# Optimization experiments

Measured on AMD Instinct MI355X. Metric: run time of the kernel, lower is better.

## Reference

```python
import jax, jax.numpy as jnp
import numpy as np

N_EMBD = 448
HEAD_SIZE = 64

def setup_inputs() -> dict:
    key = jax.random.key(0)
    k1, k2, k3, k4 = jax.random.split(key, 4)
    B, T = 16, 2048
    x = jax.random.normal(k1, (B, T, N_EMBD), dtype=jnp.float32)
    # nn.Linear(n_embd, head_size, bias=False): weight shape (head_size, n_embd); y = x @ W.T
    s = 1.0 / np.sqrt(N_EMBD)
    Wk = jax.random.uniform(k2, (HEAD_SIZE, N_EMBD), jnp.float32, -s, s)
    Wq = jax.random.uniform(k3, (HEAD_SIZE, N_EMBD), jnp.float32, -s, s)
    Wv = jax.random.uniform(k4, (HEAD_SIZE, N_EMBD), jnp.float32, -s, s)
    return {"x": x, "Wk": Wk, "Wq": Wq, "Wv": Wv}

def reference(x, Wk, Wq, Wv):
    B, T, C = x.shape
    k = jnp.einsum('btc,hc->bth', x, Wk)  # (B,T,H)
    q = jnp.einsum('btc,hc->bth', x, Wq)
    v = jnp.einsum('btc,hc->bth', x, Wv)
    scale = 1.0 / jnp.sqrt(jnp.float32(C))  # NOTE: scales by sqrt(n_embd), as in source
    wei = jnp.einsum('bth,bsh->bts', q, k) * scale  # (B,T,T)
    causal = jnp.tril(jnp.ones((T, T), dtype=bool))
    wei = jnp.where(causal[None, :, :], wei, -jnp.inf)
    wei = jax.nn.softmax(wei, axis=-1)
    # dropout is identity in eval mode
    out = jnp.einsum('bts,bsh->bth', wei, v)  # (B,T,H)
    return out
```

## Files before the change

kernel.cpp:

```cpp
#include <hip/hip_runtime.h>
#include <math.h>

#define BT 32768
#define NC 448
#define NH 64
#define TT 2048

typedef __bf16 bf16x8 __attribute__((ext_vector_type(8)));
typedef __bf16 bf16x2 __attribute__((ext_vector_type(2)));
typedef float  f32x4  __attribute__((ext_vector_type(4)));

__device__ __forceinline__ unsigned short f2bf(float f) {
  __bf16 h = (__bf16)f;
  return __builtin_bit_cast(unsigned short, h);
}
__device__ __forceinline__ ushort4 f2bf4(float4 v) {
  ushort4 b; b.x = f2bf(v.x); b.y = f2bf(v.y); b.z = f2bf(v.z); b.w = f2bf(v.w);
  return b;
}
__device__ __forceinline__ float bf2f(unsigned short u) {
  return __builtin_bit_cast(float, (unsigned)u << 16);
}


__global__ __launch_bounds__(256) void wprep_kernel(
    const float* __restrict__ Wk, const float* __restrict__ Wq,
    const float* __restrict__ Wv, unsigned short* __restrict__ wp)
{
  int idx = blockIdx.x * 256 + threadIdx.x;
  int r = idx & 63;
  int t = idx >> 6;
  int g = t & 7; t >>= 3;
  int ch = t % 7, p = t / 7;
  const float* W = (p == 0) ? Wk : ((p == 1) ? Wq : Wv);
  const float* src = &W[(size_t)r * NC + ch * 64 + g * 8];
  float4 a = *(const float4*)src;
  float4 b = *(const float4*)(src + 4);
  *(ushort4*)&wp[(size_t)idx * 8]     = f2bf4(a);
  *(ushort4*)&wp[(size_t)idx * 8 + 4] = f2bf4(b);
}

__global__ __launch_bounds__(256) void proj_kernel(
    const float* __restrict__ x, const unsigned short* __restrict__ wp,
    unsigned short* __restrict__ kws, unsigned short* __restrict__ qws,
    unsigned short* __restrict__ vws)
{
  __shared__ unsigned short xs[2][4096];
  const int tid = threadIdx.x;
  const int w = tid >> 6, lane = tid & 63;
  const int q = lane >> 4, l15 = lane & 15;
  const int r0 = blockIdx.x * 64;

  f32x4 acc[3][4];
#pragma unroll
  for (int p = 0; p < 3; ++p)
#pragma unroll
    for (int t = 0; t < 4; ++t) acc[p][t] = f32x4{0.f, 0.f, 0.f, 0.f};

  const int c0 = (tid & 15) * 4, r_ = tid >> 4;
  const int wbase = (w * 16 + l15) * 8;

  float4 xr[4];
  bf16x8 wfr[3][2], wnx[3][2];
#pragma unroll
  for (int i = 0; i < 4; ++i)
    xr[i] = *(const float4*)&x[(size_t)(r0 + r_ + 16 * i) * NC + c0];
#pragma unroll
  for (int p = 0; p < 3; ++p)
#pragma unroll
    for (int ks = 0; ks < 2; ++ks)
      wfr[p][ks] = *(const bf16x8*)&wp[(size_t)((p * 7 + 0) * 8 + (q + 4 * ks)) * 512 + wbase];

  for (int ch = 0; ch < 7; ++ch) {
    const int cur = ch & 1;
#pragma unroll
    for (int i = 0; i < 4; ++i) {
      int r = r_ + 16 * i;
      int off = r * 64 + (((c0 >> 3) ^ (r & 7)) << 3) + (c0 & 7);
      *(ushort4*)&xs[cur][off] = f2bf4(xr[i]);
    }
    __syncthreads();
    if (ch < 6) {
      int kc = (ch + 1) * 64;
#pragma unroll
      for (int i = 0; i < 4; ++i)
        xr[i] = *(const float4*)&x[(size_t)(r0 + r_ + 16 * i) * NC + kc + c0];
#pragma unroll
      for (int p = 0; p < 3; ++p)
#pragma unroll
        for (int ks = 0; ks < 2; ++ks)
          wnx[p][ks] = *(const bf16x8*)&wp[(size_t)((p * 7 + ch + 1) * 8 + (q + 4 * ks)) * 512 + wbase];
    }
#pragma unroll
    for (int ks = 0; ks < 2; ++ks) {
#pragma unroll
      for (int t = 0; t < 4; ++t) {
        int xrow = t * 16 + l15;
        bf16x8 xf = *(const bf16x8*)&xs[cur][xrow * 64 + (((q + 4 * ks) ^ (xrow & 7)) << 3)];
        acc[0][t] = __builtin_amdgcn_mfma_f32_16x16x32_bf16(wfr[0][ks], xf, acc[0][t], 0, 0, 0);
        acc[1][t] = __builtin_amdgcn_mfma_f32_16x16x32_bf16(xf, wfr[1][ks], acc[1][t], 0, 0, 0);
        acc[2][t] = __builtin_amdgcn_mfma_f32_16x16x32_bf16(xf, wfr[2][ks], acc[2][t], 0, 0, 0);
      }
    }
    if (ch < 6) {
#pragma unroll
      for (int p = 0; p < 3; ++p)
#pragma unroll
        for (int ks = 0; ks < 2; ++ks)
          wfr[p][ks] = wnx[p][ks];
    }
  }

  const size_t tile = (size_t)blockIdx.x * 4096;
#pragma unroll
  for (int t = 0; t < 4; ++t) {
    int j = t * 16 + l15;
    ushort4 bb; bb.x = f2bf(acc[0][t][0]); bb.y = f2bf(acc[0][t][1]);
    bb.z = f2bf(acc[0][t][2]); bb.w = f2bf(acc[0][t][3]);
    *(ushort4*)&kws[tile + j * 64 + (((2 * w + (q >> 1)) ^ (j & 7)) << 3) + ((q & 1) << 2)] = bb;
  }
  {
    const float qs = 0.068161075f;
    int h = w * 16 + l15;
#pragma unroll
    for (int t = 0; t < 4; ++t)
#pragma unroll
      for (int rr = 0; rr < 4; ++rr) {
        int R = r0 + t * 16 + q * 4 + rr;
        qws[(size_t)R * 64 + h] = f2bf(acc[1][t][rr] * qs);
      }
  }
  {
    int h = w * 16 + l15;
#pragma unroll
    for (int t = 0; t < 4; ++t) {
      ushort4 bb; bb.x = f2bf(acc[2][t][0]); bb.y = f2bf(acc[2][t][1]);
      bb.z = f2bf(acc[2][t][2]); bb.w = f2bf(acc[2][t][3]);
      *(ushort4*)&vws[tile + h * 64 + (((2 * t + (q >> 1)) ^ (h & 7)) << 3) + ((q & 1) << 2)] = bb;
    }
  }
}

__global__ __launch_bounds__(256) void attn_partial(
    const unsigned short* __restrict__ kws, const unsigned short* __restrict__ qws,
    const unsigned short* __restrict__ vws, float* __restrict__ out,
    unsigned short* __restrict__ opart, float* __restrict__ mlpart)
{
  __shared__ unsigned short ksm[2][4096];
  __shared__ unsigned short vtm[2][4096];
  const int bx = blockIdx.x, b = blockIdx.y;
  int qt = 0, c = 0;
  {
    int idx = bx;
    if (idx < 52) {
      for (int q2 = 31; q2 >= 7; --q2) {
        int L = (q2 + 1) >> 3;
        if (idx < L) { qt = q2; c = idx; break; }
        idx -= L;
      }
    } else {
      idx -= 52;
      for (int q2 = 31; q2 >= 0; --q2) {
        if ((q2 + 1) & 7) {
          if (idx == 0) { qt = q2; c = (q2 + 1) >> 3; break; }
          --idx;
        }
      }
    }
  }
  const int kt0 = c * 8;
  const int ktn = min(kt0 + 8, qt + 1);
  const int nt = ktn - kt0;
  const bool direct = (qt <= 7);

  const int tid = threadIdx.x;
  const int w = tid >> 6, lane = tid & 63;
  const int q = lane >> 4, l15 = lane & 15;
  const int t0 = b * TT + qt * 64;

  bf16x8 qf[2];
#pragma unroll
  for (int ks = 0; ks < 2; ++ks)
    qf[ks] = *(const bf16x8*)&qws[(size_t)(t0 + w * 16 + l15) * 64 + 32 * ks + q * 8];

  f32x4 oacc[4];
#pragma unroll
  for (int ht = 0; ht < 4; ++ht) oacc[ht] = f32x4{0.f, 0.f, 0.f, 0.f};
  float m_i = -INFINITY, l_i = 0.f;

  uint4 kr0, kr1, vr0, vr1;
  {
    const unsigned short* kt_ = kws + (size_t)(b * 32 + kt0) * 4096;
    const unsigned short* vt_ = vws + (size_t)(b * 32 + kt0) * 4096;
    kr0 = *(const uint4*)&kt_[tid * 8];  kr1 = *(const uint4*)&kt_[2048 + tid * 8];
    vr0 = *(const uint4*)&vt_[tid * 8];  vr1 = *(const uint4*)&vt_[2048 + tid * 8];
  }

  const int srcA = (((2 * q) & 3) << 4) + l15;
  const int srcB = (((2 * q + 1) & 3) << 4) + l15;
  const bool hiq = (q >> 1) != 0;

  for (int it = 0; it < nt; ++it) {
    const int kt = kt0 + it;
    const int cur = it & 1;
    *(uint4*)&ksm[cur][tid * 8] = kr0;  *(uint4*)&ksm[cur][2048 + tid * 8] = kr1;
    *(uint4*)&vtm[cur][tid * 8] = vr0;  *(uint4*)&vtm[cur][2048 + tid * 8] = vr1;
    __syncthreads();
    if (it + 1 < nt) {
      const unsigned short* kt_ = kws + (size_t)(b * 32 + kt + 1) * 4096;
      const unsigned short* vt_ = vws + (size_t)(b * 32 + kt + 1) * 4096;
      kr0 = *(const uint4*)&kt_[tid * 8];  kr1 = *(const uint4*)&kt_[2048 + tid * 8];
      vr0 = *(const uint4*)&vt_[tid * 8];  vr1 = *(const uint4*)&vt_[2048 + tid * 8];
    }

    f32x4 sacc[4];
#pragma unroll
    for (int jt = 0; jt < 4; ++jt) sacc[jt] = f32x4{0.f, 0.f, 0.f, 0.f};
    __builtin_amdgcn_s_setprio(1);
#pragma unroll
    for (int jt = 0; jt < 4; ++jt) {
      int j = jt * 16 + l15;
#pragma unroll
      for (int ks = 0; ks < 2; ++ks) {
        bf16x8 kf = *(const bf16x8*)&ksm[cur][j * 64 + (((q + 4 * ks) ^ (j & 7)) << 3)];
        sacc[jt] = __builtin_amdgcn_mfma_f32_16x16x32_bf16(kf, qf[ks], sacc[jt], 0, 0, 0);
      }
    }
    __builtin_amdgcn_s_setprio(0);

    if (kt == qt) {
      int iloc = w * 16 + l15;
#pragma unroll
      for (int jt = 0; jt < 4; ++jt)
#pragma unroll
        for (int rr = 0; rr < 4; ++rr)
          if (jt * 16 + q * 4 + rr > iloc) sacc[jt][rr] = -INFINITY;
    }

    float mx = -INFINITY;
#pragma unroll
    for (int jt = 0; jt < 4; ++jt)
#pragma unroll
      for (int rr = 0; rr < 4; ++rr) mx = fmaxf(mx, sacc[jt][rr]);
    mx = fmaxf(mx, __shfl_xor(mx, 16));
    mx = fmaxf(mx, __shfl_xor(mx, 32));
    if (!__all(mx <= m_i + 11.0f)) {
      float mn = fmaxf(m_i, mx);
      float alpha = exp2f(m_i - mn);
      m_i = mn;
      l_i *= alpha;
      float a_t[4];
#pragma unroll
      for (int rr = 0; rr < 4; ++rr) a_t[rr] = __shfl(alpha, q * 4 + rr);
#pragma unroll
      for (int ht = 0; ht < 4; ++ht)
#pragma unroll
        for (int rr = 0; rr < 4; ++rr) oacc[ht][rr] *= a_t[rr];
    }
    float rs = 0.f;
#pragma unroll
    for (int jt = 0; jt < 4; ++jt)
#pragma unroll
      for (int rr = 0; rr < 4; ++rr) {
        float pv = exp2f(sacc[jt][rr] - m_i);
        sacc[jt][rr] = pv; rs += pv;
      }
    rs += __shfl_xor(rs, 16);
    rs += __shfl_xor(rs, 32);
    l_i += rs;

    unsigned pku[4][2];
#pragma unroll
    for (int jt = 0; jt < 4; ++jt)
#pragma unroll
      for (int h2 = 0; h2 < 2; ++h2) {
        bf16x2 tpk;
        tpk[0] = (__bf16)sacc[jt][2 * h2];
        tpk[1] = (__bf16)sacc[jt][2 * h2 + 1];
        pku[jt][h2] = __builtin_bit_cast(unsigned, tpk);
      }

    __builtin_amdgcn_s_setprio(1);
#pragma unroll
    for (int ks2 = 0; ks2 < 2; ++ks2) {
      unsigned a0 = __shfl(pku[2 * ks2][0], srcA), b0 = __shfl(pku[2 * ks2 + 1][0], srcA);
      unsigned a1 = __shfl(pku[2 * ks2][1], srcA), b1 = __shfl(pku[2 * ks2 + 1][1], srcA);
      unsigned a2 = __shfl(pku[2 * ks2][0], srcB), b2 = __shfl(pku[2 * ks2 + 1][0], srcB);
      unsigned a3 = __shfl(pku[2 * ks2][1], srcB), b3 = __shfl(pku[2 * ks2 + 1][1], srcB);
      uint4 wds;
      wds.x = hiq ? b0 : a0; wds.y = hiq ? b1 : a1;
      wds.z = hiq ? b2 : a2; wds.w = hiq ? b3 : a3;
      bf16x8 pf = __builtin_bit_cast(bf16x8, wds);
#pragma unroll
      for (int ht = 0; ht < 4; ++ht) {
        int h = ht * 16 + l15;
        bf16x8 vf = *(const bf16x8*)&vtm[cur][h * 64 + (((q + 4 * ks2) ^ (h & 7)) << 3)];
        oacc[ht] = __builtin_amdgcn_mfma_f32_16x16x32_bf16(pf, vf, oacc[ht], 0, 0, 0);
      }
    }
    __builtin_amdgcn_s_setprio(0);
  }

  if (direct) {
    float l_t[4];
#pragma unroll
    for (int rr = 0; rr < 4; ++rr) l_t[rr] = __shfl(l_i, q * 4 + rr);
#pragma unroll
    for (int rr = 0; rr < 4; ++rr) {
      float inv = 1.f / l_t[rr];
      int R = t0 + w * 16 + q * 4 + rr;
#pragma unroll
      for (int ht = 0; ht < 4; ++ht)
        out[(size_t)R * 64 + ht * 16 + l15] = oacc[ht][rr] * inv;
    }
  } else {
    const int pre = (qt < 16) ? 2 * (qt - 8) : (qt < 24 ? 16 + 3 * (qt - 16) : 40 + 4 * (qt - 24));
    const size_t slot = (size_t)b * 72 + pre + c;
    unsigned short* Op = opart + slot * 4096;
#pragma unroll
    for (int rr = 0; rr < 4; ++rr) {
      int rloc = w * 16 + q * 4 + rr;
#pragma unroll
      for (int ht = 0; ht < 4; ++ht)
        Op[rloc * 64 + ht * 16 + l15] = f2bf(oacc[ht][rr]);
    }
    if (q == 0) {
      mlpart[slot * 128 + w * 16 + l15]      = m_i;
      mlpart[slot * 128 + 64 + w * 16 + l15] = l_i;
    }
  }
}

__global__ __launch_bounds__(256) void combine_kernel(
    const unsigned short* __restrict__ opart, const float* __restrict__ mlpart,
    float* __restrict__ out)
{
  const int qtc = blockIdx.x, b = blockIdx.y;
  const int qt = 8 + qtc;
  const int nc = (qt >> 3) + 1;
  const int pre = (qt < 16) ? 2 * (qt - 8) : (qt < 24 ? 16 + 3 * (qt - 16) : 40 + 4 * (qt - 24));
  const size_t s0 = (size_t)b * 72 + pre;
  const int t = threadIdx.x;
  const int r = t >> 2, c0 = (t & 3) * 16;

  float m = -INFINITY;
  for (int i = 0; i < nc; ++i)
    m = fmaxf(m, mlpart[(s0 + i) * 128 + r]);
  float wsum = 0.f;
  for (int i = 0; i < nc; ++i)
    wsum += exp2f(mlpart[(s0 + i) * 128 + r] - m) * mlpart[(s0 + i) * 128 + 64 + r];
  const float inv = 1.f / wsum;

  float res[16];
#pragma unroll
  for (int u = 0; u < 16; ++u) res[u] = 0.f;
  for (int i = 0; i < nc; ++i) {
    float wi = exp2f(mlpart[(s0 + i) * 128 + r] - m) * inv;
    const unsigned short* O = opart + (s0 + i) * 4096 + r * 64 + c0;
    union { uint4 v; unsigned short e[8]; } u0, u1;
    u0.v = *(const uint4*)&O[0];
    u1.v = *(const uint4*)&O[8];
#pragma unroll
    for (int u = 0; u < 8; ++u) {
      res[u]     += wi * bf2f(u0.e[u]);
      res[8 + u] += wi * bf2f(u1.e[u]);
    }
  }
  float* op = out + (size_t)(b * TT + qt * 64 + r) * 64 + c0;
  *(float4*)&op[0]  = make_float4(res[0], res[1], res[2], res[3]);
  *(float4*)&op[4]  = make_float4(res[4], res[5], res[6], res[7]);
  *(float4*)&op[8]  = make_float4(res[8], res[9], res[10], res[11]);
  *(float4*)&op[12] = make_float4(res[12], res[13], res[14], res[15]);
}

extern "C" void kernel_launch(void* const* d_in, const int* in_sizes, int n_in,
                              void* d_out, int out_size, void* d_ws, size_t ws_size,
                              hipStream_t stream) {
  const float* x  = (const float*)d_in[0];
  const float* Wk = (const float*)d_in[1];
  const float* Wq = (const float*)d_in[2];
  const float* Wv = (const float*)d_in[3];
  unsigned short* kws = (unsigned short*)d_ws;
  unsigned short* qws = kws + (size_t)BT * NH;
  unsigned short* vws = qws + (size_t)BT * NH;
  unsigned short* opart = vws + (size_t)BT * NH;
  float* mlpart = (float*)(opart + (size_t)1152 * 4096);
  float* out = (float*)d_out;
  unsigned short* wprep = opart;

  wprep_kernel<<<dim3(42), 256, 0, stream>>>(Wk, Wq, Wv, wprep);
  proj_kernel<<<dim3(512), 256, 0, stream>>>(x, wprep, kws, qws, vws);
  attn_partial<<<dim3(80, 16), 256, 0, stream>>>(kws, qws, vws, out, opart, mlpart);
  combine_kernel<<<dim3(24, 16), 256, 0, stream>>>(opart, mlpart, out);
}
```

Baseline: 141.3 us.

## Split attention blocks into single-wave blocks loading K/V fragments directly from global

Each 256-thread attention block becomes four independent 64-thread blocks, one per 16-row query slice. The LDS staging and __syncthreads of K/V tiles are dropped, and each wave loads its MFMA K and V fragments straight from global memory into registers, double-buffered with a ping-pong unrolled loop. The projection kernel now writes K and V without the XOR swizzle to match the new access pattern. This removes block-level barriers and LDS traffic, but each wave now reads whole K/V tiles itself, which quadruples global/L2 reads and raises register pressure.

```diff
diff --git a/kernel.cpp b/kernel.cpp
--- a/kernel.cpp
+++ b/kernel.cpp
@@ -21,7 +21,6 @@
 __device__ __forceinline__ float bf2f(unsigned short u) {
   return __builtin_bit_cast(float, (unsigned)u << 16);
 }
-
 
 __global__ __launch_bounds__(256) void wprep_kernel(
     const float* __restrict__ Wk, const float* __restrict__ Wq,
@@ -117,7 +116,7 @@
     int j = t * 16 + l15;
     ushort4 bb; bb.x = f2bf(acc[0][t][0]); bb.y = f2bf(acc[0][t][1]);
     bb.z = f2bf(acc[0][t][2]); bb.w = f2bf(acc[0][t][3]);
-    *(ushort4*)&kws[tile + j * 64 + (((2 * w + (q >> 1)) ^ (j & 7)) << 3) + ((q & 1) << 2)] = bb;
+    *(ushort4*)&kws[tile + j * 64 + w * 16 + 4 * q] = bb;
   }
   {
     const float qs = 0.068161075f;
@@ -136,22 +135,121 @@
     for (int t = 0; t < 4; ++t) {
       ushort4 bb; bb.x = f2bf(acc[2][t][0]); bb.y = f2bf(acc[2][t][1]);
       bb.z = f2bf(acc[2][t][2]); bb.w = f2bf(acc[2][t][3]);
-      *(ushort4*)&vws[tile + h * 64 + (((2 * t + (q >> 1)) ^ (h & 7)) << 3) + ((q & 1) << 2)] = bb;
-    }
-  }
-}
-
-__global__ __launch_bounds__(256) void attn_partial(
+      *(ushort4*)&vws[tile + h * 64 + t * 16 + 4 * q] = bb;
+    }
+  }
+}
+
+__device__ __forceinline__ void attn_iter(
+    bf16x8 (&kc)[4][2], bf16x8 (&vc)[4][2],
+    bf16x8 (&kn)[4][2], bf16x8 (&vn)[4][2],
+    int it, int nt, bool isdiag,
+    const unsigned short* __restrict__ kbn, const unsigned short* __restrict__ vbn,
+    const bf16x8 (&qf)[2], f32x4 (&oacc)[4],
+    float& m_i, float& l_i,
+    int q, int l15, int wv, int srcA, int srcB, bool hiq)
+{
+  if (it + 1 < nt) {
+#pragma unroll
+    for (int jt = 0; jt < 4; ++jt)
+#pragma unroll
+      for (int ks = 0; ks < 2; ++ks) {
+        kn[jt][ks] = *(const bf16x8*)&kbn[(jt * 16 + l15) * 64 + (q + 4 * ks) * 8];
+        vn[jt][ks] = *(const bf16x8*)&vbn[(jt * 16 + l15) * 64 + (q + 4 * ks) * 8];
+      }
+  }
+
+  f32x4 sacc[4];
+#pragma unroll
+  for (int jt = 0; jt < 4; ++jt) sacc[jt] = f32x4{0.f, 0.f, 0.f, 0.f};
+  __builtin_amdgcn_s_setprio(1);
+#pragma unroll
+  for (int jt = 0; jt < 4; ++jt)
+#pragma unroll
+    for (int ks = 0; ks < 2; ++ks)
+      sacc[jt] = __builtin_amdgcn_mfma_f32_16x16x32_bf16(kc[jt][ks], qf[ks], sacc[jt], 0, 0, 0);
+  __builtin_amdgcn_s_setprio(0);
+
+  if (isdiag) {
+    int iloc = wv * 16 + l15;
+#pragma unroll
+    for (int jt = 0; jt < 4; ++jt)
+#pragma unroll
+      for (int rr = 0; rr < 4; ++rr)
+        if (jt * 16 + q * 4 + rr > iloc) sacc[jt][rr] = -INFINITY;
+  }
+
+  float mx = -INFINITY;
+#pragma unroll
+  for (int jt = 0; jt < 4; ++jt)
+#pragma unroll
+    for (int rr = 0; rr < 4; ++rr) mx = fmaxf(mx, sacc[jt][rr]);
+  mx = fmaxf(mx, __shfl_xor(mx, 16));
+  mx = fmaxf(mx, __shfl_xor(mx, 32));
+  if (!__all(mx <= m_i + 11.0f)) {
+    float mn = fmaxf(m_i, mx);
+    float alpha = exp2f(m_i - mn);
+    m_i = mn;
+    l_i *= alpha;
+    float a_t[4];
+#pragma unroll
+    for (int rr = 0; rr < 4; ++rr) a_t[rr] = __shfl(alpha, q * 4 + rr);
+#pragma unroll
+    for (int ht = 0; ht < 4; ++ht)
+#pragma unroll
+      for (int rr = 0; rr < 4; ++rr) oacc[ht][rr] *= a_t[rr];
+  }
+  float rs = 0.f;
+#pragma unroll
+  for (int jt = 0; jt < 4; ++jt)
+#pragma unroll
+    for (int rr = 0; rr < 4; ++rr) {
+      float pv = exp2f(sacc[jt][rr] - m_i);
+      sacc[jt][rr] = pv; rs += pv;
+    }
+  rs += __shfl_xor(rs, 16);
+  rs += __shfl_xor(rs, 32);
+  l_i += rs;
+
+  unsigned pku[4][2];
+#pragma unroll
+  for (int jt = 0; jt < 4; ++jt)
+#pragma unroll
+    for (int h2 = 0; h2 < 2; ++h2) {
+      bf16x2 tpk;
+      tpk[0] = (__bf16)sacc[jt][2 * h2];
+      tpk[1] = (__bf16)sacc[jt][2 * h2 + 1];
+      pku[jt][h2] = __builtin_bit_cast(unsigned, tpk);
+    }
+
+  __builtin_amdgcn_s_setprio(1);
+#pragma unroll
+  for (int ks2 = 0; ks2 < 2; ++ks2) {
+    unsigned a0 = __shfl(pku[2 * ks2][0], srcA), b0 = __shfl(pku[2 * ks2 + 1][0], srcA);
+    unsigned a1 = __shfl(pku[2 * ks2][1], srcA), b1 = __shfl(pku[2 * ks2 + 1][1], srcA);
+    unsigned a2 = __shfl(pku[2 * ks2][0], srcB), b2 = __shfl(pku[2 * ks2 + 1][0], srcB);
+    unsigned a3 = __shfl(pku[2 * ks2][1], srcB), b3 = __shfl(pku[2 * ks2 + 1][1], srcB);
+    uint4 wds;
+    wds.x = hiq ? b0 : a0; wds.y = hiq ? b1 : a1;
+    wds.z = hiq ? b2 : a2; wds.w = hiq ? b3 : a3;
+    bf16x8 pf = __builtin_bit_cast(bf16x8, wds);
+#pragma unroll
+    for (int ht = 0; ht < 4; ++ht)
+      oacc[ht] = __builtin_amdgcn_mfma_f32_16x16x32_bf16(pf, vc[ht][ks2], oacc[ht], 0, 0, 0);
+  }
+  __builtin_amdgcn_s_setprio(0);
+}
+
+__global__ __launch_bounds__(64, 2) void attn_partial(
     const unsigned short* __restrict__ kws, const unsigned short* __restrict__ qws,
     const unsigned short* __restrict__ vws, float* __restrict__ out,
     unsigned short* __restrict__ opart, float* __restrict__ mlpart)
 {
-  __shared__ unsigned short ksm[2][4096];
-  __shared__ unsigned short vtm[2][4096];
   const int bx = blockIdx.x, b = blockIdx.y;
+  const int cid = bx >> 2, wv = bx & 3;
   int qt = 0, c = 0;
   {
-    int idx = bx;
+    int idx = cid;
     if (idx < 52) {
       for (int q2 = 31; q2 >= 7; --q2) {
         int L = (q2 + 1) >> 3;
@@ -173,132 +271,44 @@
   const int nt = ktn - kt0;
   const bool direct = (qt <= 7);
 
-  const int tid = threadIdx.x;
-  const int w = tid >> 6, lane = tid & 63;
+  const int lane = threadIdx.x & 63;
   const int q = lane >> 4, l15 = lane & 15;
   const int t0 = b * TT + qt * 64;
 
   bf16x8 qf[2];
 #pragma unroll
   for (int ks = 0; ks < 2; ++ks)
-    qf[ks] = *(const bf16x8*)&qws[(size_t)(t0 + w * 16 + l15) * 64 + 32 * ks + q * 8];
+    qf[ks] = *(const bf16x8*)&qws[(size_t)(t0 + wv * 16 + l15) * 64 + 32 * ks + q * 8];
 
   f32x4 oacc[4];
 #pragma unroll
   for (int ht = 0; ht < 4; ++ht) oacc[ht] = f32x4{0.f, 0.f, 0.f, 0.f};
   float m_i = -INFINITY, l_i = 0.f;
-
-  uint4 kr0, kr1, vr0, vr1;
-  {
-    const unsigned short* kt_ = kws + (size_t)(b * 32 + kt0) * 4096;
-    const unsigned short* vt_ = vws + (size_t)(b * 32 + kt0) * 4096;
-    kr0 = *(const uint4*)&kt_[tid * 8];  kr1 = *(const uint4*)&kt_[2048 + tid * 8];
-    vr0 = *(const uint4*)&vt_[tid * 8];  vr1 = *(const uint4*)&vt_[2048 + tid * 8];
-  }
 
   const int srcA = (((2 * q) & 3) << 4) + l15;
   const int srcB = (((2 * q + 1) & 3) << 4) + l15;
   const bool hiq = (q >> 1) != 0;
 
-  for (int it = 0; it < nt; ++it) {
-    const int kt = kt0 + it;
-    const int cur = it & 1;
-    *(uint4*)&ksm[cur][tid * 8] = kr0;  *(uint4*)&ksm[cur][2048 + tid * 8] = kr1;
-    *(uint4*)&vtm[cur][tid * 8] = vr0;  *(uint4*)&vtm[cur][2048 + tid * 8] = vr1;
-    __syncthreads();
-    if (it + 1 < nt) {
-      const unsigned short* kt_ = kws + (size_t)(b * 32 + kt + 1) * 4096;
-      const unsigned short* vt_ = vws + (size_t)(b * 32 + kt + 1) * 4096;
-      kr0 = *(const uint4*)&kt_[tid * 8];  kr1 = *(const uint4*)&kt_[2048 + tid * 8];
-      vr0 = *(const uint4*)&vt_[tid * 8];  vr1 = *(const uint4*)&vt_[2048 + tid * 8];
-    }
-
-    f32x4 sacc[4];
-#pragma unroll
-    for (int jt = 0; jt < 4; ++jt) sacc[jt] = f32x4{0.f, 0.f, 0.f, 0.f};
-    __builtin_amdgcn_s_setprio(1);
-#pragma unroll
-    for (int jt = 0; jt < 4; ++jt) {
-      int j = jt * 16 + l15;
-#pragma unroll
-      for (int ks = 0; ks < 2; ++ks) {
-        bf16x8 kf = *(const bf16x8*)&ksm[cur][j * 64 + (((q + 4 * ks) ^ (j & 7)) << 3)];
-        sacc[jt] = __builtin_amdgcn_mfma_f32_16x16x32_bf16(kf, qf[ks], sacc[jt], 0, 0, 0);
-      }
-    }
-    __builtin_amdgcn_s_setprio(0);
-
-    if (kt == qt) {
-      int iloc = w * 16 + l15;
-#pragma unroll
-      for (int jt = 0; jt < 4; ++jt)
-#pragma unroll
-        for (int rr = 0; rr < 4; ++rr)
-          if (jt * 16 + q * 4 + rr > iloc) sacc[jt][rr] = -INFINITY;
-    }
-
-    float mx = -INFINITY;
-#pragma unroll
-    for (int jt = 0; jt < 4; ++jt)
-#pragma unroll
-      for (int rr = 0; rr < 4; ++rr) mx = fmaxf(mx, sacc[jt][rr]);
-    mx = fmaxf(mx, __shfl_xor(mx, 16));
-    mx = fmaxf(mx, __shfl_xor(mx, 32));
-    if (!__all(mx <= m_i + 11.0f)) {
-      float mn = fmaxf(m_i, mx);
-      float alpha = exp2f(m_i - mn);
-      m_i = mn;
-      l_i *= alpha;
-      float a_t[4];
-#pragma unroll
-      for (int rr = 0; rr < 4; ++rr) a_t[rr] = __shfl(alpha, q * 4 + rr);
-#pragma unroll
-      for (int ht = 0; ht < 4; ++ht)
-#pragma unroll
-        for (int rr = 0; rr < 4; ++rr) oacc[ht][rr] *= a_t[rr];
-    }
-    float rs = 0.f;
-#pragma unroll
-    for (int jt = 0; jt < 4; ++jt)
-#pragma unroll
-      for (int rr = 0; rr < 4; ++rr) {
-        float pv = exp2f(sacc[jt][rr] - m_i);
-        sacc[jt][rr] = pv; rs += pv;
-      }
-    rs += __shfl_xor(rs, 16);
-    rs += __shfl_xor(rs, 32);
-    l_i += rs;
-
-    unsigned pku[4][2];
-#pragma unroll
-    for (int jt = 0; jt < 4; ++jt)
-#pragma unroll
-      for (int h2 = 0; h2 < 2; ++h2) {
-        bf16x2 tpk;
-        tpk[0] = (__bf16)sacc[jt][2 * h2];
-        tpk[1] = (__bf16)sacc[jt][2 * h2 + 1];
-        pku[jt][h2] = __builtin_bit_cast(unsigned, tpk);
-      }
-
-    __builtin_amdgcn_s_setprio(1);
-#pragma unroll
-    for (int ks2 = 0; ks2 < 2; ++ks2) {
-      unsigned a0 = __shfl(pku[2 * ks2][0], srcA), b0 = __shfl(pku[2 * ks2 + 1][0], srcA);
-      unsigned a1 = __shfl(pku[2 * ks2][1], srcA), b1 = __shfl(pku[2 * ks2 + 1][1], srcA);
-      unsigned a2 = __shfl(pku[2 * ks2][0], srcB), b2 = __shfl(pku[2 * ks2 + 1][0], srcB);
-      unsigned a3 = __shfl(pku[2 * ks2][1], srcB), b3 = __shfl(pku[2 * ks2 + 1][1], srcB);
-      uint4 wds;
-      wds.x = hiq ? b0 : a0; wds.y = hiq ? b1 : a1;
-      wds.z = hiq ? b2 : a2; wds.w = hiq ? b3 : a3;
-      bf16x8 pf = __builtin_bit_cast(bf16x8, wds);
-#pragma unroll
-      for (int ht = 0; ht < 4; ++ht) {
-        int h = ht * 16 + l15;
-        bf16x8 vf = *(const bf16x8*)&vtm[cur][h * 64 + (((q + 4 * ks2) ^ (h & 7)) << 3)];
-        oacc[ht] = __builtin_amdgcn_mfma_f32_16x16x32_bf16(pf, vf, oacc[ht], 0, 0, 0);
-      }
-    }
-    __builtin_amdgcn_s_setprio(0);
+  const unsigned short* kb0 = kws + (size_t)(b * 32 + kt0) * 4096;
+  const unsigned short* vb0 = vws + (size_t)(b * 32 + kt0) * 4096;
+
+  bf16x8 kA[4][2], vA[4][2], kB[4][2], vB[4][2];
+#pragma unroll
+  for (int jt = 0; jt < 4; ++jt)
+#pragma unroll
+    for (int ks = 0; ks < 2; ++ks) {
+      kA[jt][ks] = *(const bf16x8*)&kb0[(jt * 16 + l15) * 64 + (q + 4 * ks) * 8];
+      vA[jt][ks] = *(const bf16x8*)&vb0[(jt * 16 + l15) * 64 + (q + 4 * ks) * 8];
+    }
+
+  for (int it = 0; it < nt; it += 2) {
+    attn_iter(kA, vA, kB, vB, it, nt, kt0 + it == qt,
+              kb0 + (size_t)(it + 1) * 4096, vb0 + (size_t)(it + 1) * 4096,
+              qf, oacc, m_i, l_i, q, l15, wv, srcA, srcB, hiq);
+    if (it + 1 < nt)
+      attn_iter(kB, vB, kA, vA, it + 1, nt, kt0 + it + 1 == qt,
+                kb0 + (size_t)(it + 2) * 4096, vb0 + (size_t)(it + 2) * 4096,
+                qf, oacc, m_i, l_i, q, l15, wv, srcA, srcB, hiq);
   }
 
   if (direct) {
@@ -308,7 +318,7 @@
 #pragma unroll
     for (int rr = 0; rr < 4; ++rr) {
       float inv = 1.f / l_t[rr];
-      int R = t0 + w * 16 + q * 4 + rr;
+      int R = t0 + wv * 16 + q * 4 + rr;
 #pragma unroll
       for (int ht = 0; ht < 4; ++ht)
         out[(size_t)R * 64 + ht * 16 + l15] = oacc[ht][rr] * inv;
@@ -319,14 +329,14 @@
     unsigned short* Op = opart + slot * 4096;
 #pragma unroll
     for (int rr = 0; rr < 4; ++rr) {
-      int rloc = w * 16 + q * 4 + rr;
+      int rloc = wv * 16 + q * 4 + rr;
 #pragma unroll
       for (int ht = 0; ht < 4; ++ht)
         Op[rloc * 64 + ht * 16 + l15] = f2bf(oacc[ht][rr]);
     }
     if (q == 0) {
-      mlpart[slot * 128 + w * 16 + l15]      = m_i;
-      mlpart[slot * 128 + 64 + w * 16 + l15] = l_i;
+      mlpart[slot * 128 + wv * 16 + l15]      = m_i;
+      mlpart[slot * 128 + 64 + wv * 16 + l15] = l_i;
     }
   }
 }
@@ -390,6 +400,6 @@
 
   wprep_kernel<<<dim3(42), 256, 0, stream>>>(Wk, Wq, Wv, wprep);
   proj_kernel<<<dim3(512), 256, 0, stream>>>(x, wprep, kws, qws, vws);
-  attn_partial<<<dim3(80, 16), 256, 0, stream>>>(kws, qws, vws, out, opart, mlpart);
+  attn_partial<<<dim3(320, 16), 64, 0, stream>>>(kws, qws, vws, out, opart, mlpart);
   combine_kernel<<<dim3(24, 16), 256, 0, stream>>>(opart, mlpart, out);
 }
```

New measurement: 181.9 us. 28.8% more time.
